# Kernel optimization log

Measured on AMD Instinct MI355X. Metric: run time of the kernel, lower is better.

Reference implementation:

```python
import jax, jax.numpy as jnp
import numpy as np

B, N, V, H = 8, 512, 8000, 256

def setup_inputs() -> dict:
    key = jax.random.key(0)
    ks = jax.random.split(key, 7)
    scale = 0.05  # 'random_normal' initializer default stddev
    return {
        "inputs": jax.random.uniform(ks[0], (B, N, V), dtype=jnp.float32),
        "emb_w": jax.random.normal(ks[1], (V, H), dtype=jnp.float32) * scale,
        "emb_b": jnp.zeros((H,), dtype=jnp.float32),
        "wx": jax.random.normal(ks[2], (H, H), dtype=jnp.float32) * scale,
        "wh": jax.random.normal(ks[3], (H, H), dtype=jnp.float32) * scale,
        "hb": jnp.zeros((1, H), dtype=jnp.float32),
        "out_w": jax.random.normal(ks[4], (H, V), dtype=jnp.float32) * scale,
        "out_b": jnp.zeros((V,), dtype=jnp.float32),
    }

def reference(inputs, emb_w, emb_b, wx, wh, hb, out_w, out_b):
    # ProjectionLayer: [B,N,V] @ [V,H] + b -> [B,N,H]
    x = jnp.einsum("bnv,vh->bnh", inputs, emb_w) + emb_b
    b_, _, h_dim = x.shape
    # HiddenLayer: h_t = tanh(h_{t-1} @ wh + x_t @ wx + b), h_0 = 0; only final h returned
    xs = jnp.swapaxes(x, 0, 1)  # [N,B,H] time-major for scan
    h0 = jnp.zeros((b_, h_dim), dtype=x.dtype)
    def step(h, xt):
        h_new = jnp.tanh(h @ wh + xt @ wx + hb)  # [B,H]
        return h_new, None
    hT, _ = jax.lax.scan(step, h0, xs)
    hT = hT[:, None, :]  # original reshapes each step to [B,1,H]
    # Dense(V) + Softmax over last axis -> [B,1,V]
    logits = hT @ out_w + out_b
    return jax.nn.softmax(logits, axis=-1)
```

## Files before the change

kernel.cpp:

```cpp
#include <hip/hip_runtime.h>
#include <cmath>


typedef float f32x4 __attribute__((ext_vector_type(4)));
typedef __bf16 bf16x8 __attribute__((ext_vector_type(8)));

#define BM 64
#define BN 256
#define BK 64
#define KSPLIT 5
#define KCH 1600
#define NITER 25

__global__ __launch_bounds__(256) void k_transpose_bf16(const float* __restrict__ in,
                                                        __bf16* __restrict__ out,
                                                        int R, int C) {
  __shared__ __bf16 lt[64][72];
  const int tid = threadIdx.x;
  const int r0 = blockIdx.x * 64, c0 = blockIdx.y * 64;
  {
    const int rr = tid >> 2, cg = (tid & 3) * 16;
    const float* src = &in[(size_t)(r0 + rr) * C + c0 + cg];
#pragma unroll
    for (int u = 0; u < 16; u += 4) {
      f32x4 v = *(const f32x4*)(src + u);
      lt[rr][cg + u + 0] = (__bf16)v[0];
      lt[rr][cg + u + 1] = (__bf16)v[1];
      lt[rr][cg + u + 2] = (__bf16)v[2];
      lt[rr][cg + u + 3] = (__bf16)v[3];
    }
  }
  __syncthreads();
  {
    const int cc = tid >> 2, rg = (tid & 3) * 16;
    bf16x8 o0, o1;
#pragma unroll
    for (int e = 0; e < 8; ++e) o0[e] = lt[rg + e][cc];
#pragma unroll
    for (int e = 0; e < 8; ++e) o1[e] = lt[rg + 8 + e][cc];
    __bf16* dst = &out[(size_t)(c0 + cc) * R + r0 + rg];
    *(bf16x8*)(dst) = o0;
    *(bf16x8*)(dst + 8) = o1;
  }
}

__global__ __launch_bounds__(512) void k_embed_gemm(const float* __restrict__ inp,
                                                    const __bf16* __restrict__ embT,
                                                    float* __restrict__ part) {
  __shared__ __bf16 sA[BM * BK];
  __shared__ __bf16 sB[BN * BK];
  const int tid = threadIdx.x;
  const int m0 = blockIdx.x * BM;
  const int kc = blockIdx.y;
  const size_t kbase0 = (size_t)kc * KCH;
  const int lane = tid & 63;
  const int w = tid >> 6;
  const int wm = w >> 2, wn = w & 3;
  const int l16 = lane & 15, lk = lane >> 4;

  const int ar = tid >> 3, ac = (tid & 7) * 8;
  const int bc = tid >> 1, bk = (tid & 1) * 32;

  f32x4 acc[2][4] = {};

  const float* aptr = &inp[(size_t)(m0 + ar) * 8000 + kbase0 + ac];
  const __bf16* bptr = &embT[(size_t)bc * 8000 + kbase0 + bk];
  f32x4 a0 = *(const f32x4*)(aptr);
  f32x4 a1 = *(const f32x4*)(aptr + 4);
  bf16x8 b0 = *(const bf16x8*)(bptr);
  bf16x8 b1 = *(const bf16x8*)(bptr + 8);
  bf16x8 b2 = *(const bf16x8*)(bptr + 16);
  bf16x8 b3 = *(const bf16x8*)(bptr + 24);

  const int aswz = (ar & 7) << 3;
  const int bswz = (bc & 7) << 3;

  for (int it = 0; it < NITER; ++it) {
    __syncthreads();
    bf16x8 aw;
    aw[0] = (__bf16)a0[0]; aw[1] = (__bf16)a0[1]; aw[2] = (__bf16)a0[2]; aw[3] = (__bf16)a0[3];
    aw[4] = (__bf16)a1[0]; aw[5] = (__bf16)a1[1]; aw[6] = (__bf16)a1[2]; aw[7] = (__bf16)a1[3];
    *(bf16x8*)&sA[(ar * BK + ac) ^ aswz] = aw;
    *(bf16x8*)&sB[(bc * BK + bk + 0) ^ bswz] = b0;
    *(bf16x8*)&sB[(bc * BK + bk + 8) ^ bswz] = b1;
    *(bf16x8*)&sB[(bc * BK + bk + 16) ^ bswz] = b2;
    *(bf16x8*)&sB[(bc * BK + bk + 24) ^ bswz] = b3;
    __syncthreads();

    if (it + 1 < NITER) {
      const float* ap = aptr + (size_t)(it + 1) * BK;
      const __bf16* bp = bptr + (size_t)(it + 1) * BK;
      a0 = *(const f32x4*)(ap);
      a1 = *(const f32x4*)(ap + 4);
      b0 = *(const bf16x8*)(bp);
      b1 = *(const bf16x8*)(bp + 8);
      b2 = *(const bf16x8*)(bp + 16);
      b3 = *(const bf16x8*)(bp + 24);
    }

#pragma unroll
    for (int s = 0; s < 2; ++s) {
      bf16x8 af[2], bfb[4];
#pragma unroll
      for (int i = 0; i < 2; ++i) {
        const int r = wm * 32 + i * 16 + l16;
        af[i] = *(const bf16x8*)&sA[(r * BK + s * 32 + lk * 8) ^ ((r & 7) << 3)];
      }
#pragma unroll
      for (int j = 0; j < 4; ++j) {
        const int c = wn * 64 + j * 16 + l16;
        bfb[j] = *(const bf16x8*)&sB[(c * BK + s * 32 + lk * 8) ^ ((c & 7) << 3)];
      }
#pragma unroll
      for (int i = 0; i < 2; ++i)
#pragma unroll
        for (int j = 0; j < 4; ++j)
          acc[i][j] = __builtin_amdgcn_mfma_f32_16x16x32_bf16(af[i], bfb[j], acc[i][j], 0, 0, 0);
    }
  }

#pragma unroll
  for (int i = 0; i < 2; ++i)
#pragma unroll
    for (int j = 0; j < 4; ++j) {
#pragma unroll
      for (int e = 0; e < 4; ++e) {
        const int gr = m0 + wm * 32 + i * 16 + lk * 4 + e;
        const int gc = wn * 64 + j * 16 + l16;
        part[((size_t)kc * 4096 + gr) * 256 + gc] = acc[i][j][e];
      }
    }
}

#define RW_MT 16
__global__ __launch_bounds__(256) void k_reduce_wx(const float* __restrict__ part,
                                                   const float* __restrict__ emb_b,
                                                   const float* __restrict__ wx,
                                                   const float* __restrict__ hb,
                                                   float* __restrict__ xw4) {
  __shared__ float xs[RW_MT][256];
  const int m0 = blockIdx.x * RW_MT;
  const int h = threadIdx.x;
  const float eb = emb_b[h];
#pragma unroll
  for (int mi = 0; mi < RW_MT; ++mi) {
    float s = eb;
#pragma unroll
    for (int c = 0; c < KSPLIT; ++c) s += part[((size_t)c * 4096 + m0 + mi) * 256 + h];
    xs[mi][h] = s;
  }
  __syncthreads();
  float acc[RW_MT];
  const float hbv = hb[h];
#pragma unroll
  for (int mi = 0; mi < RW_MT; ++mi) acc[mi] = hbv;
  for (int k = 0; k < 256; k += 4) {
    const float w0 = wx[(k + 0) * 256 + h];
    const float w1 = wx[(k + 1) * 256 + h];
    const float w2 = wx[(k + 2) * 256 + h];
    const float w3 = wx[(k + 3) * 256 + h];
#pragma unroll
    for (int mi = 0; mi < RW_MT; ++mi) {
      f32x4 xv = *(const f32x4*)&xs[mi][k];
      acc[mi] += xv[0] * w0 + xv[1] * w1 + xv[2] * w2 + xv[3] * w3;
    }
  }
#pragma unroll
  for (int mi = 0; mi < RW_MT; ++mi) {
    const int m = m0 + mi;
    const int b = m >> 9, t = m & 511;
    xw4[((size_t)b * 512 + t) * 256 + h] = acc[mi];
  }
}

__global__ __launch_bounds__(256, 1) void k_rnn_scan(const __bf16* __restrict__ whT,
                                                     const float* __restrict__ xw4,
                                                     float* __restrict__ hT) {
  __shared__ __bf16 h2[2][256];
  const int tid = threadIdx.x;
  const int lane = tid & 63;
  const int w = tid >> 6;
  const int l16 = lane & 15, lk = lane >> 4;
  const int b = blockIdx.x;
  const bool act = (l16 == 0);
  const bool oact = (lk == 0);
  const int colb = w * 64 + l16;

  bf16x8 whB[4][8];
#pragma unroll
  for (int j = 0; j < 4; ++j) {
    const int col = colb + j * 16;
#pragma unroll
    for (int s = 0; s < 8; ++s)
      whB[j][s] = *(const bf16x8*)&whT[(size_t)col * 256 + s * 32 + lk * 8];
  }

  h2[0][tid] = (__bf16)0.0f;

  const float* xwb = &xw4[(size_t)b * 512 * 256];
  float xvA[4], xvB[4], nA[4], nB[4];
#pragma unroll
  for (int j = 0; j < 4; ++j) {
    xvA[j] = xwb[0 * 256 + colb + j * 16];
    xvB[j] = xwb[1 * 256 + colb + j * 16];
  }

  bf16x8 af[8];
#pragma unroll
  for (int s = 0; s < 8; ++s) af[s] = bf16x8{};

  __syncthreads();

#define RNN_STEP(RD, WR, XV, LAST_T)                                              \
  {                                                                               \
    if (act) {                                                                    \
      _Pragma("unroll") for (int s = 0; s < 8; ++s)                               \
          af[s] = *(const bf16x8*)&h2[RD][s * 32 + lk * 8];                       \
    }                                                                             \
    float hn[4];                                                                  \
    _Pragma("unroll") for (int j = 0; j < 4; ++j) {                               \
      f32x4 pA = {}, pB = {};                                                     \
      pA[0] = oact ? (XV)[j] : 0.0f;                                              \
      pA = __builtin_amdgcn_mfma_f32_16x16x32_bf16(af[0], whB[j][0], pA, 0, 0, 0);\
      pB = __builtin_amdgcn_mfma_f32_16x16x32_bf16(af[1], whB[j][1], pB, 0, 0, 0);\
      pA = __builtin_amdgcn_mfma_f32_16x16x32_bf16(af[2], whB[j][2], pA, 0, 0, 0);\
      pB = __builtin_amdgcn_mfma_f32_16x16x32_bf16(af[3], whB[j][3], pB, 0, 0, 0);\
      pA = __builtin_amdgcn_mfma_f32_16x16x32_bf16(af[4], whB[j][4], pA, 0, 0, 0);\
      pB = __builtin_amdgcn_mfma_f32_16x16x32_bf16(af[5], whB[j][5], pB, 0, 0, 0);\
      pA = __builtin_amdgcn_mfma_f32_16x16x32_bf16(af[6], whB[j][6], pA, 0, 0, 0);\
      pB = __builtin_amdgcn_mfma_f32_16x16x32_bf16(af[7], whB[j][7], pB, 0, 0, 0);\
      const float v = pA[0] + pB[0];                                              \
      const float e2 = __builtin_amdgcn_exp2f(v * 2.8853900817779268f);           \
      hn[j] = __builtin_fmaf(-2.0f, __builtin_amdgcn_rcpf(e2 + 1.0f), 1.0f);      \
    }                                                                             \
    if (oact) {                                                                   \
      _Pragma("unroll") for (int j = 0; j < 4; ++j) {                             \
        h2[WR][colb + j * 16] = (__bf16)hn[j];                                    \
        if (LAST_T) hT[b * 256 + colb + j * 16] = hn[j];                          \
      }                                                                           \
    }                                                                             \
    asm volatile("s_waitcnt lgkmcnt(0)" ::: "memory");                            \
    __builtin_amdgcn_sched_barrier(0);                                            \
    __builtin_amdgcn_s_barrier();                                                 \
    __builtin_amdgcn_sched_barrier(0);                                            \
  }

  for (int tt = 0; tt < 256; ++tt) {
    const int t0 = tt * 2;
    const bool more = (tt < 255);
    if (more) {
#pragma unroll
      for (int j = 0; j < 4; ++j) nA[j] = xwb[(size_t)(t0 + 2) * 256 + colb + j * 16];
    }
    RNN_STEP(0, 1, xvA, false)
    if (more) {
#pragma unroll
      for (int j = 0; j < 4; ++j) nB[j] = xwb[(size_t)(t0 + 3) * 256 + colb + j * 16];
    }
    RNN_STEP(1, 0, xvB, (tt == 255))
    if (more) {
#pragma unroll
      for (int j = 0; j < 4; ++j) { xvA[j] = nA[j]; xvB[j] = nB[j]; }
    }
  }
#undef RNN_STEP
}

__global__ __launch_bounds__(256) void k_logits(const float* __restrict__ hT,
                                                const float* __restrict__ out_w,
                                                const float* __restrict__ out_b,
                                                float* __restrict__ logits) {
  __shared__ float hs[256];
  const int vc = blockIdx.x, b = blockIdx.y;
  const int tid = threadIdx.x;
  hs[tid] = hT[b * 256 + tid];
  __syncthreads();

  const int v0 = vc * 1024 + tid * 4;
  if (v0 >= 8000) return;
  f32x4 acc = *(const f32x4*)&out_b[v0];
#pragma unroll 4
  for (int k = 0; k < 256; ++k) {
    acc += hs[k] * (*(const f32x4*)&out_w[(size_t)k * 8000 + v0]);
  }
  *(f32x4*)&logits[(size_t)b * 8192 + v0] = acc;
}

__global__ __launch_bounds__(1024) void k_softmax8(const float* __restrict__ logits,
                                                   float* __restrict__ out) {
  __shared__ float red[16];
  const int b = blockIdx.x;
  const int tid = threadIdx.x;
  const bool active = tid < 1000;
  const int v0 = tid * 8;
  f32x4 acc0 = {}, acc1 = {};
  if (active) {
    acc0 = *(const f32x4*)&logits[(size_t)b * 8192 + v0];
    acc1 = *(const f32x4*)&logits[(size_t)b * 8192 + v0 + 4];
  }

  float m = -__builtin_huge_valf();
  if (active) {
#pragma unroll
    for (int e = 0; e < 4; ++e) m = fmaxf(m, fmaxf(acc0[e], acc1[e]));
  }
#pragma unroll
  for (int off = 32; off > 0; off >>= 1) m = fmaxf(m, __shfl_xor(m, off));
  if ((tid & 63) == 0) red[tid >> 6] = m;
  __syncthreads();
  if (tid < 64) {
    float t = (tid < 16) ? red[tid] : -__builtin_huge_valf();
#pragma unroll
    for (int off = 8; off > 0; off >>= 1) t = fmaxf(t, __shfl_xor(t, off));
    if (tid == 0) red[0] = t;
  }
  __syncthreads();
  const float M = red[0];

  f32x4 e0 = {}, e1 = {};
  float s = 0.0f;
  if (active) {
#pragma unroll
    for (int e = 0; e < 4; ++e) {
      e0[e] = __expf(acc0[e] - M);
      e1[e] = __expf(acc1[e] - M);
      s += e0[e] + e1[e];
    }
  }
#pragma unroll
  for (int off = 32; off > 0; off >>= 1) s += __shfl_xor(s, off);
  if ((tid & 63) == 0) red[tid >> 6] = s;
  __syncthreads();
  if (tid < 64) {
    float t = (tid < 16) ? red[tid] : 0.0f;
#pragma unroll
    for (int off = 8; off > 0; off >>= 1) t += __shfl_xor(t, off);
    if (tid == 0) red[0] = t;
  }
  __syncthreads();
  const float inv = 1.0f / red[0];

  if (active) {
    float* op = &out[(size_t)b * 8000 + v0];
    *(f32x4*)(op) = e0 * inv;
    *(f32x4*)(op + 4) = e1 * inv;
  }
}

extern "C" void kernel_launch(void* const* d_in, const int* in_sizes, int n_in,
                              void* d_out, int out_size, void* d_ws, size_t ws_size,
                              hipStream_t stream) {
  const float* inputs = (const float*)d_in[0];
  const float* emb_w  = (const float*)d_in[1];
  const float* emb_b  = (const float*)d_in[2];
  const float* wx     = (const float*)d_in[3];
  const float* wh     = (const float*)d_in[4];
  const float* hb     = (const float*)d_in[5];
  const float* out_w  = (const float*)d_in[6];
  const float* out_b  = (const float*)d_in[7];
  float* out = (float*)d_out;

  char* ws = (char*)d_ws;
  __bf16* embT  = (__bf16*)(ws + 0);
  __bf16* whT   = (__bf16*)(ws + 4096000);
  float* part   = (float*)(ws + 4227072);
  float* xw4    = (float*)(ws + 25198592);
  float* hT     = (float*)(ws + 29392896);
  float* logits = (float*)(ws + 29401088);

  k_transpose_bf16<<<dim3(125, 4), 256, 0, stream>>>(emb_w, embT, 8000, 256);
  k_transpose_bf16<<<dim3(4, 4), 256, 0, stream>>>(wh, whT, 256, 256);
  k_embed_gemm<<<dim3(64, KSPLIT), 512, 0, stream>>>(inputs, embT, part);
  k_reduce_wx<<<256, 256, 0, stream>>>(part, emb_b, wx, hb, xw4);
  k_rnn_scan<<<8, 256, 0, stream>>>(whT, xw4, hT);
  k_logits<<<dim3(8, 8), 256, 0, stream>>>(hT, out_w, out_b, logits);
  k_softmax8<<<8, 1024, 0, stream>>>(logits, out);
}
```

Baseline: 618.2 us.

## Fold wx into embedding weights and double-buffer the embedding GEMM

Precomputes emb_w @ wx as a bf16 matrix, plus a constant bias vector emb_b @ wx + hb. The big input GEMM then produces the recurrence input directly, and the per-token wx GEMM in the reduce kernel is removed. The embedding GEMM switches to 32-row tiles with double-buffered shared memory and prefetching two stages ahead. The RNN scan is split into two launches of 256 steps, with the hidden state passed through hT in between; the logits loop unroll is also raised. The trade-offs are an extra small weight-side GEMM, an extra launch, a bf16 round-trip of the intermediate hidden state, and different rounding from applying the fused weight in bf16.

```diff
diff --git a/kernel.cpp b/kernel.cpp
--- a/kernel.cpp
+++ b/kernel.cpp
@@ -3,11 +3,9 @@
 
 
 typedef float f32x4 __attribute__((ext_vector_type(4)));
+typedef __bf16 bf16x4 __attribute__((ext_vector_type(4)));
 typedef __bf16 bf16x8 __attribute__((ext_vector_type(8)));
 
-#define BM 64
-#define BN 256
-#define BK 64
 #define KSPLIT 5
 #define KCH 1600
 #define NITER 25
@@ -44,138 +42,203 @@
   }
 }
 
-__global__ __launch_bounds__(512) void k_embed_gemm(const float* __restrict__ inp,
-                                                    const __bf16* __restrict__ embT,
-                                                    float* __restrict__ part) {
-  __shared__ __bf16 sA[BM * BK];
-  __shared__ __bf16 sB[BN * BK];
-  const int tid = threadIdx.x;
-  const int m0 = blockIdx.x * BM;
+__global__ __launch_bounds__(512) void k_w2m(const __bf16* __restrict__ wxT,
+                                             const float* __restrict__ emb_w,
+                                             __bf16* __restrict__ w2t) {
+  __shared__ __bf16 sA[256 * 64];
+  __shared__ __bf16 sB[64 * 64];
+  const int tid = threadIdx.x;
+  const int v0 = blockIdx.x * 64;
+  const int lane = tid & 63;
+  const int w = tid >> 6;
+  const int wm = w >> 1, wn = w & 1;
+  const int l16 = lane & 15, lk = lane >> 4;
+
+  const int arow = tid >> 1, aks = (tid & 1) * 32;
+  const int br = tid >> 3, bkc = (tid & 7) * 8;
+
+  f32x4 acc[4][2] = {};
+
+  for (int it = 0; it < 4; ++it) {
+    const int kb = it * 64;
+    __syncthreads();
+    {
+      const __bf16* ap = &wxT[(size_t)arow * 256 + kb + aks];
+      const int wbase = (arow * 64 + aks);
+      const int sw = (arow & 7) << 3;
+#pragma unroll
+      for (int m = 0; m < 4; ++m)
+        *(bf16x8*)&sA[(wbase + m * 8) ^ sw] = *(const bf16x8*)(ap + m * 8);
+      const float* bp = &emb_w[(size_t)(v0 + br) * 256 + kb + bkc];
+      f32x4 x0 = *(const f32x4*)(bp);
+      f32x4 x1 = *(const f32x4*)(bp + 4);
+      bf16x8 bw;
+      bw[0] = (__bf16)x0[0]; bw[1] = (__bf16)x0[1]; bw[2] = (__bf16)x0[2]; bw[3] = (__bf16)x0[3];
+      bw[4] = (__bf16)x1[0]; bw[5] = (__bf16)x1[1]; bw[6] = (__bf16)x1[2]; bw[7] = (__bf16)x1[3];
+      *(bf16x8*)&sB[(br * 64 + bkc) ^ ((br & 7) << 3)] = bw;
+    }
+    __syncthreads();
+#pragma unroll
+    for (int s = 0; s < 2; ++s) {
+      bf16x8 af[4], bfr[2];
+#pragma unroll
+      for (int i = 0; i < 4; ++i) {
+        const int r = wm * 64 + i * 16 + l16;
+        af[i] = *(const bf16x8*)&sA[(r * 64 + s * 32 + lk * 8) ^ ((r & 7) << 3)];
+      }
+#pragma unroll
+      for (int j = 0; j < 2; ++j) {
+        const int c = wn * 32 + j * 16 + l16;
+        bfr[j] = *(const bf16x8*)&sB[(c * 64 + s * 32 + lk * 8) ^ ((c & 7) << 3)];
+      }
+#pragma unroll
+      for (int i = 0; i < 4; ++i)
+#pragma unroll
+        for (int j = 0; j < 2; ++j)
+          acc[i][j] = __builtin_amdgcn_mfma_f32_16x16x32_bf16(af[i], bfr[j], acc[i][j], 0, 0, 0);
+    }
+  }
+
+#pragma unroll
+  for (int i = 0; i < 4; ++i)
+#pragma unroll
+    for (int j = 0; j < 2; ++j)
+#pragma unroll
+      for (int e = 0; e < 4; ++e) {
+        const int h = wm * 64 + i * 16 + lk * 4 + e;
+        const int v = v0 + wn * 32 + j * 16 + l16;
+        w2t[(size_t)h * 8000 + v] = (__bf16)acc[i][j][e];
+      }
+}
+
+__global__ __launch_bounds__(256) void k_c2(const float* __restrict__ emb_b,
+                                            const float* __restrict__ wx,
+                                            const float* __restrict__ hb,
+                                            float* __restrict__ c2) {
+  const int h = threadIdx.x;
+  float s = hb[h];
+#pragma unroll 8
+  for (int k = 0; k < 256; ++k) s += emb_b[k] * wx[k * 256 + h];
+  c2[h] = s;
+}
+
+__global__ __launch_bounds__(512) void k_embed_gemm2(const float* __restrict__ inp,
+                                                     const __bf16* __restrict__ w2t,
+                                                     float* __restrict__ part) {
+  __shared__ __bf16 sA[2][32 * 64];
+  __shared__ __bf16 sB[2][256 * 64];
+  const int tid = threadIdx.x;
+  const int m0 = blockIdx.x * 32;
   const int kc = blockIdx.y;
-  const size_t kbase0 = (size_t)kc * KCH;
+  const size_t kbase = (size_t)kc * KCH;
   const int lane = tid & 63;
   const int w = tid >> 6;
   const int wm = w >> 2, wn = w & 3;
   const int l16 = lane & 15, lk = lane >> 4;
 
-  const int ar = tid >> 3, ac = (tid & 7) * 8;
+  const int ar = tid >> 4, ac = (tid & 15) * 4;
   const int bc = tid >> 1, bk = (tid & 1) * 32;
-
-  f32x4 acc[2][4] = {};
-
-  const float* aptr = &inp[(size_t)(m0 + ar) * 8000 + kbase0 + ac];
-  const __bf16* bptr = &embT[(size_t)bc * 8000 + kbase0 + bk];
-  f32x4 a0 = *(const f32x4*)(aptr);
-  f32x4 a1 = *(const f32x4*)(aptr + 4);
-  bf16x8 b0 = *(const bf16x8*)(bptr);
-  bf16x8 b1 = *(const bf16x8*)(bptr + 8);
-  bf16x8 b2 = *(const bf16x8*)(bptr + 16);
-  bf16x8 b3 = *(const bf16x8*)(bptr + 24);
-
   const int aswz = (ar & 7) << 3;
   const int bswz = (bc & 7) << 3;
 
+  const float* aptr = &inp[(size_t)(m0 + ar) * 8000 + kbase + ac];
+  const __bf16* bptr = &w2t[(size_t)bc * 8000 + kbase + bk];
+
+  f32x4 acc[4] = {};
+  f32x4 a0;
+  bf16x8 b0, b1, b2, b3;
+
+  a0 = *(const f32x4*)(aptr);
+  b0 = *(const bf16x8*)(bptr);
+  b1 = *(const bf16x8*)(bptr + 8);
+  b2 = *(const bf16x8*)(bptr + 16);
+  b3 = *(const bf16x8*)(bptr + 24);
+  {
+    bf16x4 aw;
+    aw[0] = (__bf16)a0[0]; aw[1] = (__bf16)a0[1]; aw[2] = (__bf16)a0[2]; aw[3] = (__bf16)a0[3];
+    *(bf16x4*)&sA[0][(ar * 64 + ac) ^ aswz] = aw;
+    *(bf16x8*)&sB[0][(bc * 64 + bk + 0) ^ bswz] = b0;
+    *(bf16x8*)&sB[0][(bc * 64 + bk + 8) ^ bswz] = b1;
+    *(bf16x8*)&sB[0][(bc * 64 + bk + 16) ^ bswz] = b2;
+    *(bf16x8*)&sB[0][(bc * 64 + bk + 24) ^ bswz] = b3;
+  }
+  a0 = *(const f32x4*)(aptr + 64);
+  b0 = *(const bf16x8*)(bptr + 64);
+  b1 = *(const bf16x8*)(bptr + 72);
+  b2 = *(const bf16x8*)(bptr + 80);
+  b3 = *(const bf16x8*)(bptr + 88);
+  __syncthreads();
+
   for (int it = 0; it < NITER; ++it) {
-    __syncthreads();
-    bf16x8 aw;
-    aw[0] = (__bf16)a0[0]; aw[1] = (__bf16)a0[1]; aw[2] = (__bf16)a0[2]; aw[3] = (__bf16)a0[3];
-    aw[4] = (__bf16)a1[0]; aw[5] = (__bf16)a1[1]; aw[6] = (__bf16)a1[2]; aw[7] = (__bf16)a1[3];
-    *(bf16x8*)&sA[(ar * BK + ac) ^ aswz] = aw;
-    *(bf16x8*)&sB[(bc * BK + bk + 0) ^ bswz] = b0;
-    *(bf16x8*)&sB[(bc * BK + bk + 8) ^ bswz] = b1;
-    *(bf16x8*)&sB[(bc * BK + bk + 16) ^ bswz] = b2;
-    *(bf16x8*)&sB[(bc * BK + bk + 24) ^ bswz] = b3;
-    __syncthreads();
-
+    const int cur = it & 1;
     if (it + 1 < NITER) {
-      const float* ap = aptr + (size_t)(it + 1) * BK;
-      const __bf16* bp = bptr + (size_t)(it + 1) * BK;
+      bf16x4 aw;
+      aw[0] = (__bf16)a0[0]; aw[1] = (__bf16)a0[1]; aw[2] = (__bf16)a0[2]; aw[3] = (__bf16)a0[3];
+      *(bf16x4*)&sA[cur ^ 1][(ar * 64 + ac) ^ aswz] = aw;
+      *(bf16x8*)&sB[cur ^ 1][(bc * 64 + bk + 0) ^ bswz] = b0;
+      *(bf16x8*)&sB[cur ^ 1][(bc * 64 + bk + 8) ^ bswz] = b1;
+      *(bf16x8*)&sB[cur ^ 1][(bc * 64 + bk + 16) ^ bswz] = b2;
+      *(bf16x8*)&sB[cur ^ 1][(bc * 64 + bk + 24) ^ bswz] = b3;
+    }
+    if (it + 2 < NITER) {
+      const float* ap = aptr + (size_t)(it + 2) * 64;
+      const __bf16* bp = bptr + (size_t)(it + 2) * 64;
       a0 = *(const f32x4*)(ap);
-      a1 = *(const f32x4*)(ap + 4);
       b0 = *(const bf16x8*)(bp);
       b1 = *(const bf16x8*)(bp + 8);
       b2 = *(const bf16x8*)(bp + 16);
       b3 = *(const bf16x8*)(bp + 24);
     }
-
 #pragma unroll
     for (int s = 0; s < 2; ++s) {
-      bf16x8 af[2], bfb[4];
-#pragma unroll
-      for (int i = 0; i < 2; ++i) {
-        const int r = wm * 32 + i * 16 + l16;
-        af[i] = *(const bf16x8*)&sA[(r * BK + s * 32 + lk * 8) ^ ((r & 7) << 3)];
+      bf16x8 af, bfb[4];
+      {
+        const int r = wm * 16 + l16;
+        af = *(const bf16x8*)&sA[cur][(r * 64 + s * 32 + lk * 8) ^ ((r & 7) << 3)];
       }
 #pragma unroll
       for (int j = 0; j < 4; ++j) {
         const int c = wn * 64 + j * 16 + l16;
-        bfb[j] = *(const bf16x8*)&sB[(c * BK + s * 32 + lk * 8) ^ ((c & 7) << 3)];
+        bfb[j] = *(const bf16x8*)&sB[cur][(c * 64 + s * 32 + lk * 8) ^ ((c & 7) << 3)];
       }
 #pragma unroll
-      for (int i = 0; i < 2; ++i)
-#pragma unroll
-        for (int j = 0; j < 4; ++j)
-          acc[i][j] = __builtin_amdgcn_mfma_f32_16x16x32_bf16(af[i], bfb[j], acc[i][j], 0, 0, 0);
-    }
-  }
-
-#pragma unroll
-  for (int i = 0; i < 2; ++i)
-#pragma unroll
-    for (int j = 0; j < 4; ++j) {
-#pragma unroll
-      for (int e = 0; e < 4; ++e) {
-        const int gr = m0 + wm * 32 + i * 16 + lk * 4 + e;
-        const int gc = wn * 64 + j * 16 + l16;
-        part[((size_t)kc * 4096 + gr) * 256 + gc] = acc[i][j][e];
-      }
-    }
-}
-
-#define RW_MT 16
-__global__ __launch_bounds__(256) void k_reduce_wx(const float* __restrict__ part,
-                                                   const float* __restrict__ emb_b,
-                                                   const float* __restrict__ wx,
-                                                   const float* __restrict__ hb,
-                                                   float* __restrict__ xw4) {
-  __shared__ float xs[RW_MT][256];
-  const int m0 = blockIdx.x * RW_MT;
+      for (int j = 0; j < 4; ++j)
+        acc[j] = __builtin_amdgcn_mfma_f32_16x16x32_bf16(af, bfb[j], acc[j], 0, 0, 0);
+    }
+    __syncthreads();
+  }
+
+#pragma unroll
+  for (int j = 0; j < 4; ++j)
+#pragma unroll
+    for (int e = 0; e < 4; ++e) {
+      const int gr = m0 + wm * 16 + lk * 4 + e;
+      const int gc = wn * 64 + j * 16 + l16;
+      part[((size_t)kc * 4096 + gr) * 256 + gc] = acc[j][e];
+    }
+}
+
+__global__ __launch_bounds__(256) void k_reduce2(const float* __restrict__ part,
+                                                 const float* __restrict__ c2,
+                                                 float* __restrict__ xw4) {
+  const int m0 = blockIdx.x * 16;
   const int h = threadIdx.x;
-  const float eb = emb_b[h];
-#pragma unroll
-  for (int mi = 0; mi < RW_MT; ++mi) {
-    float s = eb;
-#pragma unroll
-    for (int c = 0; c < KSPLIT; ++c) s += part[((size_t)c * 4096 + m0 + mi) * 256 + h];
-    xs[mi][h] = s;
-  }
-  __syncthreads();
-  float acc[RW_MT];
-  const float hbv = hb[h];
-#pragma unroll
-  for (int mi = 0; mi < RW_MT; ++mi) acc[mi] = hbv;
-  for (int k = 0; k < 256; k += 4) {
-    const float w0 = wx[(k + 0) * 256 + h];
-    const float w1 = wx[(k + 1) * 256 + h];
-    const float w2 = wx[(k + 2) * 256 + h];
-    const float w3 = wx[(k + 3) * 256 + h];
-#pragma unroll
-    for (int mi = 0; mi < RW_MT; ++mi) {
-      f32x4 xv = *(const f32x4*)&xs[mi][k];
-      acc[mi] += xv[0] * w0 + xv[1] * w1 + xv[2] * w2 + xv[3] * w3;
-    }
-  }
-#pragma unroll
-  for (int mi = 0; mi < RW_MT; ++mi) {
+  const float cv = c2[h];
+#pragma unroll
+  for (int mi = 0; mi < 16; ++mi) {
     const int m = m0 + mi;
+    float s = cv;
+#pragma unroll
+    for (int c = 0; c < KSPLIT; ++c) s += part[((size_t)c * 4096 + m) * 256 + h];
     const int b = m >> 9, t = m & 511;
-    xw4[((size_t)b * 512 + t) * 256 + h] = acc[mi];
+    xw4[((size_t)b * 512 + t) * 256 + h] = s;
   }
 }
 
 __global__ __launch_bounds__(256, 1) void k_rnn_scan(const __bf16* __restrict__ whT,
                                                      const float* __restrict__ xw4,
-                                                     float* __restrict__ hT) {
+                                                     float* __restrict__ hT,
+                                                     int t0) {
   __shared__ __bf16 h2[2][256];
   const int tid = threadIdx.x;
   const int lane = tid & 63;
@@ -195,14 +258,14 @@
       whB[j][s] = *(const bf16x8*)&whT[(size_t)col * 256 + s * 32 + lk * 8];
   }
 
-  h2[0][tid] = (__bf16)0.0f;
+  h2[0][tid] = (t0 == 0) ? (__bf16)0.0f : (__bf16)hT[b * 256 + tid];
 
   const float* xwb = &xw4[(size_t)b * 512 * 256];
   float xvA[4], xvB[4], nA[4], nB[4];
 #pragma unroll
   for (int j = 0; j < 4; ++j) {
-    xvA[j] = xwb[0 * 256 + colb + j * 16];
-    xvB[j] = xwb[1 * 256 + colb + j * 16];
+    xvA[j] = xwb[(size_t)(t0 + 0) * 256 + colb + j * 16];
+    xvB[j] = xwb[(size_t)(t0 + 1) * 256 + colb + j * 16];
   }
 
   bf16x8 af[8];
@@ -245,19 +308,19 @@
     __builtin_amdgcn_sched_barrier(0);                                            \
   }
 
-  for (int tt = 0; tt < 256; ++tt) {
-    const int t0 = tt * 2;
-    const bool more = (tt < 255);
+  for (int tt = 0; tt < 128; ++tt) {
+    const int tg = t0 + tt * 2;
+    const bool more = (tt < 127);
     if (more) {
 #pragma unroll
-      for (int j = 0; j < 4; ++j) nA[j] = xwb[(size_t)(t0 + 2) * 256 + colb + j * 16];
+      for (int j = 0; j < 4; ++j) nA[j] = xwb[(size_t)(tg + 2) * 256 + colb + j * 16];
     }
     RNN_STEP(0, 1, xvA, false)
     if (more) {
 #pragma unroll
-      for (int j = 0; j < 4; ++j) nB[j] = xwb[(size_t)(t0 + 3) * 256 + colb + j * 16];
-    }
-    RNN_STEP(1, 0, xvB, (tt == 255))
+      for (int j = 0; j < 4; ++j) nB[j] = xwb[(size_t)(tg + 3) * 256 + colb + j * 16];
+    }
+    RNN_STEP(1, 0, xvB, (tt == 127))
     if (more) {
 #pragma unroll
       for (int j = 0; j < 4; ++j) { xvA[j] = nA[j]; xvB[j] = nB[j]; }
@@ -279,7 +342,7 @@
   const int v0 = vc * 1024 + tid * 4;
   if (v0 >= 8000) return;
   f32x4 acc = *(const f32x4*)&out_b[v0];
-#pragma unroll 4
+#pragma unroll 8
   for (int k = 0; k < 256; ++k) {
     acc += hs[k] * (*(const f32x4*)&out_w[(size_t)k * 8000 + v0]);
   }
@@ -361,18 +424,23 @@
   float* out = (float*)d_out;
 
   char* ws = (char*)d_ws;
-  __bf16* embT  = (__bf16*)(ws + 0);
-  __bf16* whT   = (__bf16*)(ws + 4096000);
-  float* part   = (float*)(ws + 4227072);
-  float* xw4    = (float*)(ws + 25198592);
-  float* hT     = (float*)(ws + 29392896);
-  float* logits = (float*)(ws + 29401088);
-
-  k_transpose_bf16<<<dim3(125, 4), 256, 0, stream>>>(emb_w, embT, 8000, 256);
+  __bf16* whT   = (__bf16*)(ws + 0);
+  __bf16* wxT   = (__bf16*)(ws + 131072);
+  __bf16* w2t   = (__bf16*)(ws + 262144);
+  float* part   = (float*)(ws + 4358144);
+  float* xw4    = (float*)(ws + 25329664);
+  float* hT     = (float*)(ws + 29523968);
+  float* c2     = (float*)(ws + 29532160);
+  float* logits = (float*)(ws + 29533184);
+
   k_transpose_bf16<<<dim3(4, 4), 256, 0, stream>>>(wh, whT, 256, 256);
-  k_embed_gemm<<<dim3(64, KSPLIT), 512, 0, stream>>>(inputs, embT, part);
-  k_reduce_wx<<<256, 256, 0, stream>>>(part, emb_b, wx, hb, xw4);
-  k_rnn_scan<<<8, 256, 0, stream>>>(whT, xw4, hT);
+  k_transpose_bf16<<<dim3(4, 4), 256, 0, stream>>>(wx, wxT, 256, 256);
+  k_w2m<<<125, 512, 0, stream>>>(wxT, emb_w, w2t);
+  k_c2<<<1, 256, 0, stream>>>(emb_b, wx, hb, c2);
+  k_embed_gemm2<<<dim3(128, KSPLIT), 512, 0, stream>>>(inputs, w2t, part);
+  k_reduce2<<<256, 256, 0, stream>>>(part, c2, xw4);
+  k_rnn_scan<<<8, 256, 0, stream>>>(whT, xw4, hT, 0);
+  k_rnn_scan<<<8, 256, 0, stream>>>(whT, xw4, hT, 256);
   k_logits<<<dim3(8, 8), 256, 0, stream>>>(hT, out_w, out_b, logits);
   k_softmax8<<<8, 1024, 0, stream>>>(logits, out);
 }
```

Measured after the change: 581.2 us. 6.0% less time.
